# Kernel tuning notes

Hardware: AMD Instinct MI355X
Metric: run time of the kernel (lower is better)

## Reference

```python
import jax, jax.numpy as jnp
import numpy as np
from jax import lax

# math_model config (baked constants)
B, DX, DY, DD = 4096, 128, 1, 128
N, ND, DT = 64, 16, 0.02
DH, L = 1024, 3
T = N + ND + 1
EPS = 1e-5


def _bn(x, g, b):
    # training-mode BatchNorm1d: biased batch stats
    m = jnp.mean(x, axis=0)
    v = jnp.var(x, axis=0)
    return (x - m) * lax.rsqrt(v + EPS) * g + b


def _driver_f(t, x_t, y_t, y_d, z_t, z_d):
    # representative delay-BSDE driver f(t, x_t, x_t, y_t, y_delay, z_t, z_delay) -> [B, DY]
    return (-y_t + 0.1 * y_d + jnp.sum(z_t * z_d, axis=-1)
            + 0.01 * jnp.sum(x_t, axis=-1, keepdims=True))


def setup_inputs() -> dict:
    key = jax.random.key(0)
    ks = jax.random.split(key, 8)
    s = 0.03
    return dict(
        x=jax.random.normal(ks[0], (B, DX, T), dtype=jnp.float32),
        dW_f=jax.random.normal(ks[1], (B, DD, 1, N), dtype=jnp.float32) * np.float32(np.sqrt(DT)),
        initial_y=jax.random.uniform(ks[2], (DY, 1), dtype=jnp.float32),
        bn_in_g=jnp.ones(2 * DX + 1, jnp.float32), bn_in_b=jnp.zeros(2 * DX + 1, jnp.float32),
        W_in=jax.random.normal(ks[3], (2 * DX + 1, DH), dtype=jnp.float32) * s,
        b_in=jnp.zeros(DH, jnp.float32),
        Ws_h=jax.random.normal(ks[4], (L, DH, DH), dtype=jnp.float32) * s,
        bs_h=jnp.zeros((L, DH), jnp.float32),
        bns_g=jnp.ones((L, DH), jnp.float32), bns_b=jnp.zeros((L, DH), jnp.float32),
        bn_out_g=jnp.ones(DH, jnp.float32), bn_out_b=jnp.zeros(DH, jnp.float32),
        W_out=jax.random.normal(ks[5], (DH, DY * DD), dtype=jnp.float32) * s,
        b_out=jnp.zeros(DY * DD, jnp.float32),
    )


def reference(x, dW_f, initial_y, bn_in_g, bn_in_b, W_in, b_in, Ws_h, bs_h,
              bns_g, bns_b, bn_out_g, bn_out_b, W_out, b_out):
    def one_pass(inpt):  # [B, 2*DX+1] -> [B, DY*DD]
        s = jnp.tanh(_bn(inpt, bn_in_g, bn_in_b) @ W_in + b_in)
        for l in range(L):
            s = jnp.tanh(_bn(s, bns_g[l], bns_b[l]) @ Ws_h[l] + bs_h[l])
        return _bn(s, bn_out_g, bn_out_b) @ W_out + b_out

    # y: [B, DY, T], first ND+1 slots = initial_y; z: [B, DY, DD, T] zeros
    y0 = jnp.zeros((B, DY, T), x.dtype).at[:, :, :ND + 1].set(initial_y[None])
    z0 = jnp.zeros((B, DY, DD, T), x.dtype)
    yt0 = jnp.broadcast_to(initial_y[:, 0][None], (B, DY))

    ones_col = jnp.ones((B, 1), x.dtype)

    def step(carry, i):
        y_t, y, z = carry
        i_t = i + ND
        t = i.astype(jnp.float32) * DT
        x_it = lax.dynamic_index_in_dim(x, i_t, 2, keepdims=False)   # [B, DX]
        x_id = lax.dynamic_index_in_dim(x, i, 2, keepdims=False)     # [B, DX]
        inpt = jnp.concatenate([x_it, x_id, ones_col * t], axis=-1)
        z_t = one_pass(inpt).reshape(B, DY, DD)
        y_d = lax.dynamic_index_in_dim(y, i, 2, keepdims=False)      # [B, DY]
        z_d = lax.dynamic_index_in_dim(z, i, 3, keepdims=False)      # [B, DY, DD]
        drv = _driver_f(t, x_it, y_t, y_d, z_t, z_d)                 # [B, DY]
        dW = lax.dynamic_index_in_dim(dW_f, i, 3, keepdims=False)    # [B, DD, 1]
        vol = jnp.matmul(z_t, dW)[..., 0]                            # [B, DY]
        y_t = y_t - drv * DT + vol
        y = lax.dynamic_update_index_in_dim(y, y_t, i_t + 1, 2)
        z = lax.dynamic_update_index_in_dim(z, z_t, i_t + 1, 3)
        return (y_t, y, z), None

    (y_t, y, z), _ = lax.scan(step, (yt0, y0, z0), jnp.arange(N))
    return y_t, y, z
```

## Files before the change

### kernel.cpp

```cpp
#include <hip/hip_runtime.h>

typedef unsigned short u16;
typedef short bhalf8 __attribute__((ext_vector_type(8)));
typedef float floatx4 __attribute__((ext_vector_type(4)));


__device__ __forceinline__ float b2f(u16 h) {
  unsigned int u = ((unsigned int)h) << 16; float f; __builtin_memcpy(&f, &u, 4); return f;
}
__device__ __forceinline__ u16 f2b(float f) {
  unsigned int u; __builtin_memcpy(&u, &f, 4);
  u = u + 0x7fffu + ((u >> 16) & 1u);
  return (u16)(u >> 16);
}
__device__ __forceinline__ float tanh_fast(float x) {
  float cx = fminf(fmaxf(x, -15.f), 15.f);
  float e = __expf(2.f * cx);
  return __fdividef(e - 1.f, e + 1.f);
}
__device__ __forceinline__ void gll16(const void* g, void* l) {
  __builtin_amdgcn_global_load_lds(
      (const __attribute__((address_space(1))) unsigned int*)g,
      (__attribute__((address_space(3))) unsigned int*)l, 16, 0, 0);
}

__global__ void xstats_partial(const float* __restrict__ x, float* __restrict__ ps, float* __restrict__ pq) {
  int p = blockIdx.x * 256 + threadIdx.x;
  int bc = blockIdx.y;
  int d = p / 80, t = p % 80;
  const float* xp = x + (size_t)d * 81 + t;
  float s = 0.f, q = 0.f;
  int b0 = bc * 256;
  for (int b = b0; b < b0 + 256; ++b) {
    float v = xp[(size_t)b * 10368];
    s += v; q += v * v;
  }
  ps[(size_t)bc * 10240 + p] = s;
  pq[(size_t)bc * 10240 + p] = q;
}

__global__ void xstats_final(const float* __restrict__ ps, const float* __restrict__ pq,
                             float* __restrict__ meanx, float* __restrict__ rstdx) {
  int p = blockIdx.x * 256 + threadIdx.x;
  float s = 0.f, q = 0.f;
  for (int c = 0; c < 16; ++c) { s += ps[(size_t)c * 10240 + p]; q += pq[(size_t)c * 10240 + p]; }
  float m = s * (1.0f / 4096.0f);
  float v = q * (1.0f / 4096.0f) - m * m;
  meanx[p] = m;
  rstdx[p] = rsqrtf(v + 1e-5f);
}

__global__ void build_inpt(const float* __restrict__ x, const float* __restrict__ meanx,
                           const float* __restrict__ rstdx, const float* __restrict__ g,
                           const float* __restrict__ bb, u16* __restrict__ inpt,
                           float* __restrict__ xs, int c0, int G) {
  __shared__ float xl[128 * 33];
  int b = blockIdx.x, tid = threadIdx.x;
  int W = G + 16;
  const float* xb = x + (size_t)b * 10368;
  for (int j = tid; j < 128 * W; j += 256) {
    int d = j / W, t = j % W;
    xl[d * 33 + t] = xb[(size_t)d * 81 + c0 + t];
  }
  __syncthreads();
  int lane = tid & 63, wid = tid >> 6;
  for (int i = wid; i < G; i += 4) {
    float s = xl[lane * 33 + i + 16] + xl[(lane + 64) * 33 + i + 16];
#pragma unroll
    for (int off = 32; off > 0; off >>= 1) s += __shfl_xor(s, off);
    if (lane == 0) xs[(size_t)(c0 + i) * 4096 + b] = 0.01f * s;
  }
  for (int i = 0; i < G; ++i) {
    u16* row = inpt + ((size_t)i * 4096 + b) * 320;
    int tt = c0 + i + 16, td = c0 + i;
    for (int col = tid; col < 320; col += 256) {
      float val;
      if (col < 128) {
        int d = col;
        val = (xl[d * 33 + i + 16] - meanx[d * 80 + tt]) * rstdx[d * 80 + tt] * g[col] + bb[col];
      } else if (col < 256) {
        int d = col - 128;
        val = (xl[d * 33 + i] - meanx[d * 80 + td]) * rstdx[d * 80 + td] * g[col] + bb[col];
      } else if (col == 256) {
        val = bb[256];
      } else {
        val = 0.f;
      }
      row[col] = f2b(val);
    }
  }
}

__global__ void transpose_win(const float* __restrict__ W, u16* __restrict__ Wt) {
  int id = blockIdx.x * 256 + threadIdx.x;
  int n = id / 320, k = id % 320;
  float v = (k < 257) ? W[(size_t)k * 1024 + n] : 0.f;
  Wt[id] = f2b(v);
}

__global__ void stats_partial_S(const u16* __restrict__ S, float* __restrict__ ps,
                                float* __restrict__ pq, int G) {
  int rc = blockIdx.x;
  int step = blockIdx.y;
  int c4 = threadIdx.x * 4;
  const u16* base = S + ((size_t)step * 4096 + (size_t)rc * 256) * 1024 + c4;
  float s0 = 0, s1 = 0, s2 = 0, s3 = 0, q0 = 0, q1 = 0, q2 = 0, q3 = 0;
#pragma unroll 4
  for (int rr = 0; rr < 256; ++rr) {
    uint2 u = *(const uint2*)(base + (size_t)rr * 1024);
    float v0 = b2f((u16)(u.x & 0xffff)), v1 = b2f((u16)(u.x >> 16));
    float v2 = b2f((u16)(u.y & 0xffff)), v3 = b2f((u16)(u.y >> 16));
    s0 += v0; q0 += v0 * v0; s1 += v1; q1 += v1 * v1;
    s2 += v2; q2 += v2 * v2; s3 += v3; q3 += v3 * v3;
  }
  size_t o = ((size_t)rc * G + step) * 1024 + c4;
  ps[o + 0] = s0; ps[o + 1] = s1; ps[o + 2] = s2; ps[o + 3] = s3;
  pq[o + 0] = q0; pq[o + 1] = q1; pq[o + 2] = q2; pq[o + 3] = q3;
}

__global__ void stats_final_S(const float* __restrict__ ps, const float* __restrict__ pq,
                              const float* __restrict__ g, const float* __restrict__ bb,
                              float* __restrict__ a_buf, float* __restrict__ c_buf, int GK) {
  int id = blockIdx.x * 256 + threadIdx.x;
  int col = id & 1023;
  float s = 0.f, q = 0.f;
  for (int rc = 0; rc < 16; ++rc) { s += ps[(size_t)rc * GK + id]; q += pq[(size_t)rc * GK + id]; }
  float m = s * (1.0f / 4096.0f);
  float v = q * (1.0f / 4096.0f) - m * m;
  float a = g[col] * rsqrtf(v + 1e-5f);
  a_buf[id] = a;
  c_buf[id] = bb[col] - m * a;
}

__global__ void scaleW(const float* __restrict__ W, const float* __restrict__ a_buf,
                       u16* __restrict__ Wt, int N, int G) {
  __shared__ float T[64][65];
  __shared__ float aa[64];
  int n0 = blockIdx.x * 64, k0 = blockIdx.y * 64;
  int tid = threadIdx.x;
  int tn = tid & 63, t4 = tid >> 6;
  for (int it = 0; it < 16; ++it) {
    int k = it * 4 + t4;
    T[tn][k] = W[(size_t)(k0 + k) * N + n0 + tn];
  }
  __syncthreads();
  int wk = tid & 63, w4 = tid >> 6;
  for (int s = 0; s < G; ++s) {
    if (tid < 64) aa[tid] = a_buf[(size_t)s * 1024 + k0 + tid];
    __syncthreads();
    u16* out = Wt + ((size_t)s * N + n0) * 1024 + k0;
    for (int it = 0; it < 16; ++it) {
      int n = it * 4 + w4;
      out[(size_t)n * 1024 + wk] = f2b(T[n][wk] * aa[wk]);
    }
    __syncthreads();
  }
}

__global__ void biasfold(const float* __restrict__ W, const float* __restrict__ c_buf,
                         const float* __restrict__ b0, float* __restrict__ bias2, int N) {
  __shared__ float cl[1024];
  int s = blockIdx.y;
  int n = blockIdx.x * blockDim.x + threadIdx.x;
  for (int j = threadIdx.x; j < 1024; j += blockDim.x) cl[j] = c_buf[(size_t)s * 1024 + j];
  __syncthreads();
  if (n < N) {
    float acc = b0[n];
#pragma unroll 4
    for (int k = 0; k < 1024; ++k) acc += cl[k] * W[(size_t)k * N + n];
    bias2[(size_t)s * N + n] = acc;
  }
}

__global__ __launch_bounds__(256, 2)
void gemm_bt(const u16* __restrict__ A, const u16* __restrict__ Bt,
             const float* __restrict__ bias, void* __restrict__ Cv,
             int K, int N, long long sB, int sBias, int flags) {
  __shared__ alignas(16) u16 As[128 * 64];
  __shared__ alignas(16) u16 Bs[128 * 64];
  const int tid = threadIdx.x;

  const int gx = gridDim.x;
  const int gxy = gx * gridDim.y;
  const int nwg = gxy * gridDim.z;
  const int orig = blockIdx.z * gxy + blockIdx.y * gx + blockIdx.x;
  const int qq = nwg >> 3, r8 = nwg & 7;
  const int xcd = orig & 7, off8 = orig >> 3;
  const int wg = (xcd < r8 ? xcd * (qq + 1) : r8 * (qq + 1) + (xcd - r8) * qq) + off8;
  const int step = wg / gxy;
  const int wrem = wg - step * gxy;
  const int m0 = (wrem / gx) * 128;
  const int n0 = (wrem % gx) * 128;

  const size_t row0 = (size_t)step * 4096 + m0;
  const u16* Ab = A + row0 * (size_t)K;
  const u16* Bb = Bt + (size_t)step * (size_t)sB + (size_t)n0 * (size_t)K;

  const u16* ag[4]; const u16* bg[4]; u16* al[4]; u16* bl[4];
#pragma unroll
  for (int j = 0; j < 4; ++j) {
    int ci = j * 256 + tid;
    int row = ci >> 3, cc = ci & 7;
    int gc = cc ^ (row & 7);
    ag[j] = Ab + (size_t)row * K + gc * 8;
    bg[j] = Bb + (size_t)row * K + gc * 8;
    al[j] = &As[ci * 8];
    bl[j] = &Bs[ci * 8];
  }

  const int lane = tid & 63, wid = tid >> 6;
  const int wm = (wid >> 1) * 64, wn = (wid & 1) * 64;
  const int q = lane >> 4, r = lane & 15;

  floatx4 zero = {0.f, 0.f, 0.f, 0.f};
  floatx4 acc[4][4];
#pragma unroll
  for (int mt = 0; mt < 4; ++mt)
#pragma unroll
    for (int nt = 0; nt < 4; ++nt) acc[mt][nt] = zero;

  int aoff[2][4], boff[2][4];
#pragma unroll
  for (int ks = 0; ks < 2; ++ks)
#pragma unroll
    for (int t = 0; t < 4; ++t) {
      int ra = wm + t * 16 + r;
      aoff[ks][t] = ra * 64 + (((ks * 4 + q) ^ (ra & 7)) * 8);
      int rb = wn + t * 16 + r;
      boff[ks][t] = rb * 64 + (((ks * 4 + q) ^ (rb & 7)) * 8);
    }

  for (int k0 = 0; k0 < K; k0 += 64) {
#pragma unroll
    for (int j = 0; j < 4; ++j) { gll16(ag[j], al[j]); ag[j] += 64; }
#pragma unroll
    for (int j = 0; j < 4; ++j) { gll16(bg[j], bl[j]); bg[j] += 64; }
    __syncthreads();
#pragma unroll
    for (int ks = 0; ks < 2; ++ks) {
      bhalf8 af[4], bf[4];
#pragma unroll
      for (int t = 0; t < 4; ++t) af[t] = *(const bhalf8*)&As[aoff[ks][t]];
#pragma unroll
      for (int t = 0; t < 4; ++t) bf[t] = *(const bhalf8*)&Bs[boff[ks][t]];
#pragma unroll
      for (int mt = 0; mt < 4; ++mt)
#pragma unroll
        for (int nt = 0; nt < 4; ++nt)
          acc[mt][nt] = __builtin_amdgcn_mfma_f32_16x16x32_bf16(af[mt], bf[nt], acc[mt][nt], 0, 0, 0);
    }
    __syncthreads();
  }

  const float* bp = bias + (size_t)step * sBias;
  if (flags & 2) {
    float* C = (float*)Cv;
#pragma unroll
    for (int nt = 0; nt < 4; ++nt) {
      int col = n0 + wn + nt * 16 + r;
      float bv = bp[col];
#pragma unroll
      for (int mt = 0; mt < 4; ++mt)
#pragma unroll
        for (int rr = 0; rr < 4; ++rr) {
          size_t row = row0 + wm + mt * 16 + q * 4 + rr;
          C[row * (size_t)N + col] = acc[mt][nt][rr] + bv;
        }
    }
  } else {
    u16* C = (u16*)Cv;
#pragma unroll
    for (int nt = 0; nt < 4; ++nt) {
      int col = n0 + wn + nt * 16 + r;
      float bv = bp[col];
#pragma unroll
      for (int mt = 0; mt < 4; ++mt)
#pragma unroll
        for (int rr = 0; rr < 4; ++rr) {
          size_t row = row0 + wm + mt * 16 + q * 4 + rr;
          C[row * (size_t)N + col] = f2b(tanh_fast(acc[mt][nt][rr] + bv));
        }
    }
  }
}

__global__ void trans_dW(const float* __restrict__ dW, float* __restrict__ dWt) {
  __shared__ float L[128 * 65];
  int b = blockIdx.x, tid = threadIdx.x;
  const float* src = dW + (size_t)b * 8192;
  for (int j = tid; j < 8192; j += 256) { int d = j >> 6, i = j & 63; L[d * 65 + i] = src[j]; }
  __syncthreads();
  for (int it = 0; it < 32; ++it) {
    int i = it * 2 + (tid >> 7), d = tid & 127;
    dWt[((size_t)i * 4096 + b) * 128 + d] = L[d * 65 + i];
  }
}

__global__ void driver_k(const float* __restrict__ Z, const float* __restrict__ dWt,
                         float* __restrict__ vol, float* __restrict__ zz) {
  int task = blockIdx.x * 4 + (threadIdx.x >> 6);
  int lane = threadIdx.x & 63;
  int b = task >> 6, i = task & 63;
  const float2* zp = (const float2*)(Z + ((size_t)i * 4096 + b) * 128) + lane;
  const float2* wp = (const float2*)(dWt + ((size_t)i * 4096 + b) * 128) + lane;
  float2 z = *zp, w = *wp;
  float pv = z.x * w.x + z.y * w.y;
  float pz = 0.f;
  if (i >= 17) {
    const float2* zd = (const float2*)(Z + ((size_t)(i - 17) * 4096 + b) * 128) + lane;
    float2 d = *zd;
    pz = z.x * d.x + z.y * d.y;
  }
#pragma unroll
  for (int off = 32; off > 0; off >>= 1) {
    pv += __shfl_xor(pv, off);
    pz += __shfl_xor(pz, off);
  }
  if (lane == 0) {
    vol[(size_t)i * 4096 + b] = pv;
    zz[(size_t)i * 4096 + b] = pz;
  }
}

__global__ void driver_slow(const float* __restrict__ Z, const float* __restrict__ dW,
                            float* __restrict__ vol, float* __restrict__ zz) {
  int task = blockIdx.x * 4 + (threadIdx.x >> 6);
  int lane = threadIdx.x & 63;
  int b = task >> 6, i = task & 63;
  const float* zp = Z + ((size_t)i * 4096 + b) * 128;
  float z0 = zp[lane], z1 = zp[lane + 64];
  float w0 = dW[(size_t)b * 8192 + (size_t)lane * 64 + i];
  float w1 = dW[(size_t)b * 8192 + (size_t)(lane + 64) * 64 + i];
  float pv = z0 * w0 + z1 * w1;
  float pz = 0.f;
  if (i >= 17) {
    const float* zd = Z + ((size_t)(i - 17) * 4096 + b) * 128;
    pz = z0 * zd[lane] + z1 * zd[lane + 64];
  }
#pragma unroll
  for (int off = 32; off > 0; off >>= 1) {
    pv += __shfl_xor(pv, off);
    pz += __shfl_xor(pz, off);
  }
  if (lane == 0) {
    vol[(size_t)i * 4096 + b] = pv;
    zz[(size_t)i * 4096 + b] = pz;
  }
}

__global__ void scan_k(const float* __restrict__ vol, const float* __restrict__ zz,
                       const float* __restrict__ xs, const float* __restrict__ y0p,
                       float* __restrict__ out) {
  int b = blockIdx.x * 256 + threadIdx.x;
  float y0 = y0p[0];
  float* yt_out = out;
  float* y_out = out + 4096;
  float yhist[64];
  float y_t = y0;
#pragma unroll
  for (int i = 0; i < 64; ++i) {
    float yd = y0;
    if (i >= 17) yd = yhist[i - 17];
    float drv = -y_t + 0.1f * yd + zz[(size_t)i * 4096 + b] + xs[(size_t)i * 4096 + b];
    y_t = y_t - drv * 0.02f + vol[(size_t)i * 4096 + b];
    yhist[i] = y_t;
    y_out[(size_t)b * 81 + i + 17] = y_t;
  }
  for (int t = 0; t < 17; ++t) y_out[(size_t)b * 81 + t] = y0;
  yt_out[b] = y_t;
}

__global__ void zout_k(const float* __restrict__ Z, float* __restrict__ outz) {
  __shared__ float L[128 * 65];
  int b = blockIdx.x, tid = threadIdx.x;
  for (int j = tid; j < 8192; j += 256) {
    int i = j >> 7, d = j & 127;
    L[d * 65 + i] = Z[((size_t)i * 4096 + b) * 128 + d];
  }
  __syncthreads();
  float* dst = outz + (size_t)b * 10368;
  for (int j = tid; j < 10368; j += 256) {
    int d = j / 81, t = j % 81;
    dst[j] = (t < 17) ? 0.f : L[d * 65 + (t - 17)];
  }
}

extern "C" void kernel_launch(void* const* d_in, const int* in_sizes, int n_in,
                              void* d_out, int out_size, void* d_ws, size_t ws_size,
                              hipStream_t stream) {
  const float* x     = (const float*)d_in[0];
  const float* dWf   = (const float*)d_in[1];
  const float* y0p   = (const float*)d_in[2];
  const float* bing  = (const float*)d_in[3];
  const float* binb  = (const float*)d_in[4];
  const float* W_in  = (const float*)d_in[5];
  const float* b_in  = (const float*)d_in[6];
  const float* Ws_h  = (const float*)d_in[7];
  const float* bs_h  = (const float*)d_in[8];
  const float* bns_g = (const float*)d_in[9];
  const float* bns_b = (const float*)d_in[10];
  const float* bog   = (const float*)d_in[11];
  const float* bob   = (const float*)d_in[12];
  const float* W_out = (const float*)d_in[13];
  const float* b_out = (const float*)d_in[14];
  float* out = (float*)d_out;

  const size_t DWTB = 134217728ull;
  const size_t PERSIST = 141000000ull;
  auto chunkB = [](int G) { return (size_t)G * 19279872ull + 262144ull; };
  int G = 16;
  while (G > 1) {
    size_t cb = chunkB(G); if (cb < DWTB) cb = DWTB;
    if (PERSIST + cb <= ws_size) break;
    G >>= 1;
  }
  size_t needFast = chunkB(G) < DWTB ? DWTB : chunkB(G);
  bool fast_dw = (PERSIST + needFast) <= ws_size;

  char* w = (char*)d_ws;
  auto alloc = [&](size_t bytes) { char* p = w; w += (bytes + 255) & ~(size_t)255; return p; };
  float* Z     = (float*)alloc(64ull * 4096 * 128 * 4);
  float* xs    = (float*)alloc(64ull * 4096 * 4);
  float* volb  = (float*)alloc(64ull * 4096 * 4);
  float* zzb   = (float*)alloc(64ull * 4096 * 4);
  float* meanx = (float*)alloc(10240 * 4);
  float* rstdx = (float*)alloc(10240 * 4);
  float* psx   = (float*)alloc(16ull * 10240 * 4);
  float* pqx   = (float*)alloc(16ull * 10240 * 4);
  u16*   Wt_i  = (u16*)alloc(1024ull * 320 * 2);
  char*  cbase = w;
  u16*   S_a   = (u16*)alloc((size_t)G * 4096 * 1024 * 2);
  u16*   S_b   = (u16*)alloc((size_t)G * 4096 * 1024 * 2);
  u16*   Wt_h  = (u16*)alloc((size_t)G * 1024 * 1024 * 2);
  u16*   Wt_o  = (u16*)alloc((size_t)G * 128 * 1024 * 2);
  float* psum  = (float*)alloc(16ull * G * 1024 * 4);
  float* pqsum = (float*)alloc(16ull * G * 1024 * 4);
  float* a_buf = (float*)alloc((size_t)G * 1024 * 4);
  float* c_buf = (float*)alloc((size_t)G * 1024 * 4);
  float* bias2 = (float*)alloc((size_t)G * 1024 * 4);
  u16*   INPT  = S_b;
  float* dWt   = (float*)cbase;

  xstats_partial<<<dim3(40, 16), 256, 0, stream>>>(x, psx, pqx);
  xstats_final<<<40, 256, 0, stream>>>(psx, pqx, meanx, rstdx);
  transpose_win<<<1280, 256, 0, stream>>>(W_in, Wt_i);

  for (int c0 = 0; c0 < 64; c0 += G) {
    build_inpt<<<4096, 256, 0, stream>>>(x, meanx, rstdx, bing, binb, INPT, xs, c0, G);
    gemm_bt<<<dim3(8, 32, G), 256, 0, stream>>>(INPT, Wt_i, b_in, S_a, 320, 1024, 0, 0, 1);
    u16* bufs[2] = {S_a, S_b};
    for (int l = 0; l < 3; ++l) {
      u16* Sin = bufs[l & 1];
      u16* Sout = bufs[(l + 1) & 1];
      const float* Wl = Ws_h + (size_t)l * 1024 * 1024;
      stats_partial_S<<<dim3(16, G), 256, 0, stream>>>(Sin, psum, pqsum, G);
      stats_final_S<<<4 * G, 256, 0, stream>>>(psum, pqsum, bns_g + l * 1024, bns_b + l * 1024, a_buf, c_buf, G * 1024);
      scaleW<<<dim3(16, 16), 256, 0, stream>>>(Wl, a_buf, Wt_h, 1024, G);
      biasfold<<<dim3(4, G), 256, 0, stream>>>(Wl, c_buf, bs_h + l * 1024, bias2, 1024);
      gemm_bt<<<dim3(8, 32, G), 256, 0, stream>>>(Sin, Wt_h, bias2, Sout, 1024, 1024, 1024ll * 1024, 1024, 1);
    }
    stats_partial_S<<<dim3(16, G), 256, 0, stream>>>(S_b, psum, pqsum, G);
    stats_final_S<<<4 * G, 256, 0, stream>>>(psum, pqsum, bog, bob, a_buf, c_buf, G * 1024);
    scaleW<<<dim3(2, 16), 256, 0, stream>>>(W_out, a_buf, Wt_o, 128, G);
    biasfold<<<dim3(1, G), 128, 0, stream>>>(W_out, c_buf, b_out, bias2, 128);
    gemm_bt<<<dim3(1, 32, G), 256, 0, stream>>>(S_b, Wt_o, bias2, Z + (size_t)c0 * 4096 * 128, 1024, 128, 128ll * 1024, 128, 2);
  }

  if (fast_dw) {
    trans_dW<<<4096, 256, 0, stream>>>(dWf, dWt);
    driver_k<<<65536, 256, 0, stream>>>(Z, dWt, volb, zzb);
  } else {
    driver_slow<<<65536, 256, 0, stream>>>(Z, dWf, volb, zzb);
  }
  scan_k<<<16, 256, 0, stream>>>(volb, zzb, xs, y0p, out);
  zout_k<<<4096, 256, 0, stream>>>(Z, out + 4096 + 4096 * 81);
}
```

Baseline: 5.323 ms.

## Fuse BatchNorm column statistics into GEMM epilogue, drop separate stats pass

The tanh GEMM epilogue now also accumulates per-column sums and sums of squares of the bf16-rounded outputs. It reduces them across lanes with shuffles and across warps in shared memory, then writes per-128-row-block partials. This removes the stats_partial_S kernels, which re-read each 4096x1024 bf16 activation matrix from memory. In exchange the GEMM epilogue gains extra arithmetic, a __syncthreads and more shared memory, and stats_final_S now reduces 32 partials instead of 16, so the workspace grows slightly.

```diff
diff --git a/kernel.cpp b/kernel.cpp
--- a/kernel.cpp
+++ b/kernel.cpp
@@ -98,33 +98,13 @@
   Wt[id] = f2b(v);
 }
 
-__global__ void stats_partial_S(const u16* __restrict__ S, float* __restrict__ ps,
-                                float* __restrict__ pq, int G) {
-  int rc = blockIdx.x;
-  int step = blockIdx.y;
-  int c4 = threadIdx.x * 4;
-  const u16* base = S + ((size_t)step * 4096 + (size_t)rc * 256) * 1024 + c4;
-  float s0 = 0, s1 = 0, s2 = 0, s3 = 0, q0 = 0, q1 = 0, q2 = 0, q3 = 0;
-#pragma unroll 4
-  for (int rr = 0; rr < 256; ++rr) {
-    uint2 u = *(const uint2*)(base + (size_t)rr * 1024);
-    float v0 = b2f((u16)(u.x & 0xffff)), v1 = b2f((u16)(u.x >> 16));
-    float v2 = b2f((u16)(u.y & 0xffff)), v3 = b2f((u16)(u.y >> 16));
-    s0 += v0; q0 += v0 * v0; s1 += v1; q1 += v1 * v1;
-    s2 += v2; q2 += v2 * v2; s3 += v3; q3 += v3 * v3;
-  }
-  size_t o = ((size_t)rc * G + step) * 1024 + c4;
-  ps[o + 0] = s0; ps[o + 1] = s1; ps[o + 2] = s2; ps[o + 3] = s3;
-  pq[o + 0] = q0; pq[o + 1] = q1; pq[o + 2] = q2; pq[o + 3] = q3;
-}
-
 __global__ void stats_final_S(const float* __restrict__ ps, const float* __restrict__ pq,
                               const float* __restrict__ g, const float* __restrict__ bb,
                               float* __restrict__ a_buf, float* __restrict__ c_buf, int GK) {
   int id = blockIdx.x * 256 + threadIdx.x;
   int col = id & 1023;
   float s = 0.f, q = 0.f;
-  for (int rc = 0; rc < 16; ++rc) { s += ps[(size_t)rc * GK + id]; q += pq[(size_t)rc * GK + id]; }
+  for (int rc = 0; rc < 32; ++rc) { s += ps[(size_t)rc * GK + id]; q += pq[(size_t)rc * GK + id]; }
   float m = s * (1.0f / 4096.0f);
   float v = q * (1.0f / 4096.0f) - m * m;
   float a = g[col] * rsqrtf(v + 1e-5f);
@@ -175,9 +155,11 @@
 __global__ __launch_bounds__(256, 2)
 void gemm_bt(const u16* __restrict__ A, const u16* __restrict__ Bt,
              const float* __restrict__ bias, void* __restrict__ Cv,
-             int K, int N, long long sB, int sBias, int flags) {
+             int K, int N, long long sB, int sBias, int flags,
+             float* __restrict__ ps, float* __restrict__ pq) {
   __shared__ alignas(16) u16 As[128 * 64];
   __shared__ alignas(16) u16 Bs[128 * 64];
+  __shared__ float sred[2][2][128];
   const int tid = threadIdx.x;
 
   const int gx = gridDim.x;
@@ -189,7 +171,8 @@
   const int wg = (xcd < r8 ? xcd * (qq + 1) : r8 * (qq + 1) + (xcd - r8) * qq) + off8;
   const int step = wg / gxy;
   const int wrem = wg - step * gxy;
-  const int m0 = (wrem / gx) * 128;
+  const int mb = wrem / gx;
+  const int m0 = mb * 128;
   const int n0 = (wrem % gx) * 128;
 
   const size_t row0 = (size_t)step * 4096 + m0;
@@ -269,6 +252,9 @@
     }
   } else {
     u16* C = (u16*)Cv;
+    float sA[4], qA[4];
+#pragma unroll
+    for (int nt = 0; nt < 4; ++nt) { sA[nt] = 0.f; qA[nt] = 0.f; }
 #pragma unroll
     for (int nt = 0; nt < 4; ++nt) {
       int col = n0 + wn + nt * 16 + r;
@@ -278,8 +264,37 @@
 #pragma unroll
         for (int rr = 0; rr < 4; ++rr) {
           size_t row = row0 + wm + mt * 16 + q * 4 + rr;
-          C[row * (size_t)N + col] = f2b(tanh_fast(acc[mt][nt][rr] + bv));
+          u16 hb = f2b(tanh_fast(acc[mt][nt][rr] + bv));
+          C[row * (size_t)N + col] = hb;
+          if (flags & 4) {
+            float vf = b2f(hb);
+            sA[nt] += vf; qA[nt] += vf * vf;
+          }
         }
+    }
+    if (flags & 4) {
+#pragma unroll
+      for (int nt = 0; nt < 4; ++nt) {
+        sA[nt] += __shfl_xor(sA[nt], 16); qA[nt] += __shfl_xor(qA[nt], 16);
+        sA[nt] += __shfl_xor(sA[nt], 32); qA[nt] += __shfl_xor(qA[nt], 32);
+      }
+      if (q == 0) {
+#pragma unroll
+        for (int nt = 0; nt < 4; ++nt) {
+          sred[wid >> 1][0][wn + nt * 16 + r] = sA[nt];
+          sred[wid >> 1][1][wn + nt * 16 + r] = qA[nt];
+        }
+      }
+      __syncthreads();
+      const int G = gridDim.z;
+      if (tid < 128) {
+        float v = sred[0][0][tid] + sred[1][0][tid];
+        ps[((size_t)mb * G + step) * (size_t)N + n0 + tid] = v;
+      } else {
+        int c = tid - 128;
+        float v = sred[0][1][c] + sred[1][1][c];
+        pq[((size_t)mb * G + step) * (size_t)N + n0 + c] = v;
+      }
     }
   }
 }
@@ -407,7 +422,7 @@
 
   const size_t DWTB = 134217728ull;
   const size_t PERSIST = 141000000ull;
-  auto chunkB = [](int G) { return (size_t)G * 19279872ull + 262144ull; };
+  auto chunkB = [](int G) { return (size_t)G * 19410944ull + 262144ull; };
   int G = 16;
   while (G > 1) {
     size_t cb = chunkB(G); if (cb < DWTB) cb = DWTB;
@@ -433,8 +448,8 @@
   u16*   S_b   = (u16*)alloc((size_t)G * 4096 * 1024 * 2);
   u16*   Wt_h  = (u16*)alloc((size_t)G * 1024 * 1024 * 2);
   u16*   Wt_o  = (u16*)alloc((size_t)G * 128 * 1024 * 2);
-  float* psum  = (float*)alloc(16ull * G * 1024 * 4);
-  float* pqsum = (float*)alloc(16ull * G * 1024 * 4);
+  float* psum  = (float*)alloc(32ull * G * 1024 * 4);
+  float* pqsum = (float*)alloc(32ull * G * 1024 * 4);
   float* a_buf = (float*)alloc((size_t)G * 1024 * 4);
   float* c_buf = (float*)alloc((size_t)G * 1024 * 4);
   float* bias2 = (float*)alloc((size_t)G * 1024 * 4);
@@ -447,23 +462,21 @@
 
   for (int c0 = 0; c0 < 64; c0 += G) {
     build_inpt<<<4096, 256, 0, stream>>>(x, meanx, rstdx, bing, binb, INPT, xs, c0, G);
-    gemm_bt<<<dim3(8, 32, G), 256, 0, stream>>>(INPT, Wt_i, b_in, S_a, 320, 1024, 0, 0, 1);
+    gemm_bt<<<dim3(8, 32, G), 256, 0, stream>>>(INPT, Wt_i, b_in, S_a, 320, 1024, 0, 0, 1 | 4, psum, pqsum);
     u16* bufs[2] = {S_a, S_b};
     for (int l = 0; l < 3; ++l) {
       u16* Sin = bufs[l & 1];
       u16* Sout = bufs[(l + 1) & 1];
       const float* Wl = Ws_h + (size_t)l * 1024 * 1024;
-      stats_partial_S<<<dim3(16, G), 256, 0, stream>>>(Sin, psum, pqsum, G);
       stats_final_S<<<4 * G, 256, 0, stream>>>(psum, pqsum, bns_g + l * 1024, bns_b + l * 1024, a_buf, c_buf, G * 1024);
       scaleW<<<dim3(16, 16), 256, 0, stream>>>(Wl, a_buf, Wt_h, 1024, G);
       biasfold<<<dim3(4, G), 256, 0, stream>>>(Wl, c_buf, bs_h + l * 1024, bias2, 1024);
-      gemm_bt<<<dim3(8, 32, G), 256, 0, stream>>>(Sin, Wt_h, bias2, Sout, 1024, 1024, 1024ll * 1024, 1024, 1);
-    }
-    stats_partial_S<<<dim3(16, G), 256, 0, stream>>>(S_b, psum, pqsum, G);
+      gemm_bt<<<dim3(8, 32, G), 256, 0, stream>>>(Sin, Wt_h, bias2, Sout, 1024, 1024, 1024ll * 1024, 1024, 1 | 4, psum, pqsum);
+    }
     stats_final_S<<<4 * G, 256, 0, stream>>>(psum, pqsum, bog, bob, a_buf, c_buf, G * 1024);
     scaleW<<<dim3(2, 16), 256, 0, stream>>>(W_out, a_buf, Wt_o, 128, G);
     biasfold<<<dim3(1, G), 128, 0, stream>>>(W_out, c_buf, b_out, bias2, 128);
-    gemm_bt<<<dim3(1, 32, G), 256, 0, stream>>>(S_b, Wt_o, bias2, Z + (size_t)c0 * 4096 * 128, 1024, 128, 128ll * 1024, 128, 2);
+    gemm_bt<<<dim3(1, 32, G), 256, 0, stream>>>(S_b, Wt_o, bias2, Z + (size_t)c0 * 4096 * 128, 1024, 128, 128ll * 1024, 128, 2, psum, pqsum);
   }
 
   if (fast_dw) {
```

Result: faster. 5.091 ms (-4.4%).
